# Performance work log

Measured on AMD Instinct MI355X. Metric: run time of the kernel, lower is better.

The kernel has to match this reference:

```python
import jax, jax.numpy as jnp
import numpy as np

NUM_HEADS = 16
HEAD_DIM = 64  # hidden_size 1024 / 16 heads


def setup_inputs() -> dict:
    key = jax.random.key(0)
    ks = jax.random.split(key, 4)
    B, S, H = 2, 2048, 1024
    scale = 1.0 / np.sqrt(H)
    return {
        "hidden_states": jax.random.normal(ks[0], (B, S, H), dtype=jnp.float32),
        "attention_mask": jnp.zeros((B, 1, 1, S), dtype=jnp.float32),
        "Wq": jax.random.normal(ks[1], (H, H), dtype=jnp.float32) * scale,
        "bq": jnp.zeros((H,), dtype=jnp.float32),
        "Wk": jax.random.normal(ks[2], (H, H), dtype=jnp.float32) * scale,
        "bk": jnp.zeros((H,), dtype=jnp.float32),
        "Wv": jax.random.normal(ks[3], (H, H), dtype=jnp.float32) * scale,
        "bv": jnp.zeros((H,), dtype=jnp.float32),
    }


def reference(hidden_states, attention_mask, Wq, bq, Wk, bk, Wv, bv):
    B, S, H = hidden_states.shape
    h, d = NUM_HEADS, HEAD_DIM

    def heads(x):  # [B,S,H] -> [B,h,S,d]
        return x.reshape(B, S, h, d).transpose(0, 2, 1, 3)

    q = heads(hidden_states @ Wq + bq)
    k = heads(hidden_states @ Wk + bk)
    v = heads(hidden_states @ Wv + bv)

    # [B,h,S,S] scores, scaled then additive-masked (HF BERT semantics)
    scores = jnp.einsum("bhqd,bhkd->bhqk", q, k) / jnp.sqrt(jnp.float32(d))
    scores = scores + attention_mask
    probs = jax.nn.softmax(scores, axis=-1)  # dropout p=0 -> identity

    ctx = jnp.einsum("bhqk,bhkd->bhqd", probs, v)
    ctx = ctx.transpose(0, 2, 1, 3).reshape(B, S, H)
    return ctx
```

## Files before the change

kernel.cpp:

```cpp
#include <hip/hip_runtime.h>
#include <hip/hip_bf16.h>


#define SEQ   2048
#define HID   1024
#define NHEAD 16
#define HD    64
#define SD    ((size_t)SEQ * HD)

typedef __bf16 bf16x8 __attribute__((ext_vector_type(8)));
typedef float  f32x4  __attribute__((ext_vector_type(4)));

#define L2E 1.4426950408889634f
#define SOFT_OFF 16.0f

__device__ __forceinline__ unsigned short f2b(float f) {
    unsigned int x = __float_as_uint(f);
    x += 0x7FFFu + ((x >> 16) & 1u);
    return (unsigned short)(x >> 16);
}

__device__ __forceinline__ void gload16(const unsigned short* g,
                                        unsigned short* l) {
    __builtin_amdgcn_global_load_lds(
        (const __attribute__((address_space(1))) unsigned int*)g,
        (__attribute__((address_space(3))) unsigned int*)l, 16, 0, 0);
}

__global__ __launch_bounds__(256) void cvt_x_k(const float* __restrict__ X,
                                               unsigned short* __restrict__ Xb)
{
    const size_t i = ((size_t)blockIdx.x * 256 + threadIdx.x) * 4;
    const float4 v = *(const float4*)(X + i);
    ushort4 o;
    o.x = f2b(v.x); o.y = f2b(v.y); o.z = f2b(v.z); o.w = f2b(v.w);
    *(ushort4*)(Xb + i) = o;
}

__global__ __launch_bounds__(256) void cvt_w_k(
    const float* __restrict__ Wq, const float* __restrict__ Wk,
    const float* __restrict__ Wv, unsigned short* __restrict__ Wtb)
{
    __shared__ __align__(16) unsigned short T[64][68];
    const int z = blockIdx.z;
    const float* __restrict__ W = (z == 0) ? Wq : (z == 1) ? Wk : Wv;
    const int k0 = blockIdx.x * 64, n0 = blockIdx.y * 64;
    const int tid = threadIdx.x;
    #pragma unroll
    for (int it = 0; it < 16; ++it) {
        const int idx = 256 * it + tid;
        const int r = idx >> 6, c = idx & 63;
        T[c][r] = f2b(W[(size_t)(k0 + r) * HID + n0 + c]);
    }
    __syncthreads();
    unsigned short* dst = Wtb + (size_t)z * HID * HID;
    #pragma unroll
    for (int it = 0; it < 4; ++it) {
        const int idx = 256 * it + tid;
        const int n = idx >> 4, c4 = (idx & 15) * 4;
        *(ushort4*)(dst + (size_t)(n0 + n) * HID + k0 + c4) = *(ushort4*)&T[n][c4];
    }
}

__device__ __forceinline__ void gemm_epilogue(
    f32x4 acc[4][4], const float* __restrict__ Bp,
    unsigned short* __restrict__ scratch, unsigned short (*Et)[68],
    int z, int m0, int n0, int wr, int wc, int ln, int quad)
{
    const int b = m0 >> 11;
    const int srow0 = (m0 + wr) & (SEQ - 1);
    const int head = (n0 + wc) >> 6;
    __syncthreads();

    if (z == 2) {
        #pragma unroll
        for (int half = 0; half < 2; ++half) {
            #pragma unroll
            for (int nt2 = 0; nt2 < 2; ++nt2) {
                const int nt = half * 2 + nt2;
                const float bias = Bp[n0 + wc + nt * 16 + ln];
                #pragma unroll
                for (int mt = 0; mt < 4; ++mt) {
                    ushort4 o;
                    o.x = f2b(acc[mt][nt][0] + bias);
                    o.y = f2b(acc[mt][nt][1] + bias);
                    o.z = f2b(acc[mt][nt][2] + bias);
                    o.w = f2b(acc[mt][nt][3] + bias);
                    *(ushort4*)&Et[nt2 * 16 + ln][mt * 16 + quad * 4] = o;
                }
            }
            __syncthreads();
            #pragma unroll
            for (int it = 0; it < 8; ++it) {
                const int d = it * 4 + quad, s4 = ln * 4;
                *(ushort4*)(scratch +
                    ((size_t)(64 + b * NHEAD + head) * HD + half * 32 + d) * SEQ
                    + srow0 + s4) = *(const ushort4*)&Et[d][s4];
            }
            __syncthreads();
        }
    } else {
        #pragma unroll
        for (int half = 0; half < 2; ++half) {
            #pragma unroll
            for (int mt2 = 0; mt2 < 2; ++mt2) {
                const int mt = half * 2 + mt2;
                #pragma unroll
                for (int nt = 0; nt < 4; ++nt) {
                    const float bias = Bp[n0 + wc + nt * 16 + ln];
                    #pragma unroll
                    for (int r = 0; r < 4; ++r)
                        Et[mt2 * 16 + quad * 4 + r][nt * 16 + ln] =
                            f2b(acc[mt][nt][r] + bias);
                }
            }
            __syncthreads();
            #pragma unroll
            for (int it = 0; it < 8; ++it) {
                const int r = it * 4 + quad, c4 = ln * 4;
                *(ushort4*)(scratch +
                    ((size_t)(z * 32 + b * NHEAD + head) * SEQ + srow0
                     + half * 32 + r) * HD + c4) = *(const ushort4*)&Et[r][c4];
            }
            __syncthreads();
        }
    }
}

__global__ __launch_bounds__(256) void qkv_gemm_bf16(
    const unsigned short* __restrict__ Xb, const unsigned short* __restrict__ Wtb,
    const float* __restrict__ bq, const float* __restrict__ bk,
    const float* __restrict__ bv, unsigned short* __restrict__ scratch)
{
    __shared__ __align__(16) unsigned short pool[2][2][128][32];

    const int z = blockIdx.z;
    const float* __restrict__ Bp = (z == 0) ? bq : (z == 1) ? bk : bv;
    const unsigned short* __restrict__ Wz = Wtb + (size_t)z * HID * HID;

    const int tid = threadIdx.x, w = tid >> 6, lane = tid & 63;
    const int ln = lane & 15, quad = lane >> 4;
    const int wr = (w >> 1) * 64, wc = (w & 1) * 64;
    const int m0 = blockIdx.x * 128, n0 = blockIdx.y * 128;

    const int L0 = w * 128 + lane;
    const int r0 = L0 >> 2,        c0 = (L0 & 3) * 8;
    const int r1 = (L0 + 64) >> 2, c1 = ((L0 + 64) & 3) * 8;

    f32x4 acc[4][4];
    #pragma unroll
    for (int i = 0; i < 4; ++i)
        #pragma unroll
        for (int j = 0; j < 4; ++j) acc[i][j] = (f32x4){0.f, 0.f, 0.f, 0.f};

    {
        unsigned short* lx = &pool[0][0][0][0] + (size_t)(w * 128) * 8;
        unsigned short* lw = &pool[0][1][0][0] + (size_t)(w * 128) * 8;
        gload16(Xb + (size_t)(m0 + r0) * HID + c0, lx);
        gload16(Xb + (size_t)(m0 + r1) * HID + c1, lx + 64 * 8);
        gload16(Wz + (size_t)(n0 + r0) * HID + c0, lw);
        gload16(Wz + (size_t)(n0 + r1) * HID + c1, lw + 64 * 8);
    }

    int cur = 0;
    for (int k0 = 0; k0 < HID; k0 += 32) {
        __syncthreads();
        if (k0 + 32 < HID) {
            const int kn = k0 + 32, nxt = cur ^ 1;
            unsigned short* lx = &pool[nxt][0][0][0] + (size_t)(w * 128) * 8;
            unsigned short* lw = &pool[nxt][1][0][0] + (size_t)(w * 128) * 8;
            gload16(Xb + (size_t)(m0 + r0) * HID + kn + c0, lx);
            gload16(Xb + (size_t)(m0 + r1) * HID + kn + c1, lx + 64 * 8);
            gload16(Wz + (size_t)(n0 + r0) * HID + kn + c0, lw);
            gload16(Wz + (size_t)(n0 + r1) * HID + kn + c1, lw + 64 * 8);
        }

        bf16x8 am[4], bn[4];
        #pragma unroll
        for (int t = 0; t < 4; ++t) {
            am[t] = *(const bf16x8*)&pool[cur][0][wr + t * 16 + ln][quad * 8];
            bn[t] = *(const bf16x8*)&pool[cur][1][wc + t * 16 + ln][quad * 8];
        }
        #pragma unroll
        for (int mt = 0; mt < 4; ++mt)
            #pragma unroll
            for (int nt = 0; nt < 4; ++nt)
                acc[mt][nt] = __builtin_amdgcn_mfma_f32_16x16x32_bf16(
                    am[mt], bn[nt], acc[mt][nt], 0, 0, 0);
        cur ^= 1;
    }
    unsigned short (*Et)[68] =
        (unsigned short (*)[68])((unsigned char*)pool + (size_t)w * 4352);
    gemm_epilogue(acc, Bp, scratch, Et, z, m0, n0, wr, wc, ln, quad);
}

__global__ __launch_bounds__(256) void qkv_gemm_fp32(
    const float* __restrict__ X,
    const float* __restrict__ Wq, const float* __restrict__ bq,
    const float* __restrict__ Wk, const float* __restrict__ bk,
    const float* __restrict__ Wv, const float* __restrict__ bv,
    unsigned short* __restrict__ scratch)
{
    __shared__ __align__(16) unsigned char pool[20480];
    unsigned short (*Xs)[40] = (unsigned short (*)[40])pool;
    unsigned short (*Wt)[40] = (unsigned short (*)[40])(pool + 10240);

    const int z = blockIdx.z;
    const float* __restrict__ W  = (z == 0) ? Wq : (z == 1) ? Wk : Wv;
    const float* __restrict__ Bp = (z == 0) ? bq : (z == 1) ? bk : bv;

    const int tid = threadIdx.x, w = tid >> 6, lane = tid & 63;
    const int ln = lane & 15, quad = lane >> 4;
    const int wr = (w >> 1) * 64, wc = (w & 1) * 64;
    const int m0 = blockIdx.x * 128, n0 = blockIdx.y * 128;

    const int xr = tid >> 3, xc = (tid & 7) * 4;
    const int wkr = tid >> 5, wnc = (tid & 31) * 4;

    f32x4 acc[4][4];
    #pragma unroll
    for (int i = 0; i < 4; ++i)
        #pragma unroll
        for (int j = 0; j < 4; ++j) acc[i][j] = (f32x4){0.f, 0.f, 0.f, 0.f};

    for (int k0 = 0; k0 < HID; k0 += 32) {
        __syncthreads();
        #pragma unroll
        for (int it = 0; it < 4; ++it) {
            const int r = xr + 32 * it;
            const float4 xv = *(const float4*)(X + (size_t)(m0 + r) * HID + k0 + xc);
            ushort4 xb;
            xb.x = f2b(xv.x); xb.y = f2b(xv.y); xb.z = f2b(xv.z); xb.w = f2b(xv.w);
            *(ushort4*)&Xs[r][xc] = xb;
            const int kr = wkr + 8 * it;
            const float4 wv = *(const float4*)(W + (size_t)(k0 + kr) * HID + n0 + wnc);
            Wt[wnc + 0][kr] = f2b(wv.x);
            Wt[wnc + 1][kr] = f2b(wv.y);
            Wt[wnc + 2][kr] = f2b(wv.z);
            Wt[wnc + 3][kr] = f2b(wv.w);
        }
        __syncthreads();
        bf16x8 am[4], bn[4];
        #pragma unroll
        for (int t = 0; t < 4; ++t) {
            am[t] = *(const bf16x8*)&Xs[wr + t * 16 + ln][quad * 8];
            bn[t] = *(const bf16x8*)&Wt[wc + t * 16 + ln][quad * 8];
        }
        #pragma unroll
        for (int mt = 0; mt < 4; ++mt)
            #pragma unroll
            for (int nt = 0; nt < 4; ++nt)
                acc[mt][nt] = __builtin_amdgcn_mfma_f32_16x16x32_bf16(
                    am[mt], bn[nt], acc[mt][nt], 0, 0, 0);
    }
    unsigned short (*Et)[68] = (unsigned short (*)[68])(pool + (size_t)w * 4352);
    gemm_epilogue(acc, Bp, scratch, Et, z, m0, n0, wr, wc, ln, quad);
}

__global__ __launch_bounds__(256) void attn_mfma(
    const unsigned short* __restrict__ scratch,
    const float* __restrict__ mask,
    float* __restrict__ out)
{
    __shared__ __align__(16) unsigned char smem[37888];
    unsigned short (*Ks)[64][72] = (unsigned short (*)[64][72])smem;
    unsigned short (*Vt)[64][72] = (unsigned short (*)[64][72])(smem + 18432);
    float* lrbuf = (float*)(smem + 36864);
    float (*OA)[68] = (float (*)[68])smem;
    float (*OB)[68] = (float (*)[68])(smem + 18432);

    const int orig = blockIdx.x;
    const int wg = ((orig & 7) << 7) + (orig >> 3);
    const int qt = wg & 31;
    const int bh = wg >> 5;
    const int b = bh >> 4, head = bh & 15;

    const unsigned short* __restrict__ Qp  = scratch + (size_t)bh * SD;
    const unsigned short* __restrict__ Kp  = scratch + (size_t)(32 + bh) * SD;
    const unsigned short* __restrict__ Vtp = scratch + (size_t)(64 + bh) * SD;
    const float* __restrict__ maskp = mask + b * SEQ;

    const int tid = threadIdx.x, w = tid >> 6, lane = tid & 63;
    const int ln = lane & 15, quad = lane >> 4;
    const int wk0 = w * 16;

    bf16x8 qb[4][2];
    #pragma unroll
    for (int t = 0; t < 4; ++t)
        #pragma unroll
        for (int h = 0; h < 2; ++h)
            qb[t][h] = *(const bf16x8*)(Qp +
                (size_t)(qt * 64 + t * 16 + ln) * HD + h * 32 + quad * 8);

    f32x4 O[4][4];
    #pragma unroll
    for (int i = 0; i < 4; ++i)
        #pragma unroll
        for (int j = 0; j < 4; ++j) O[i][j] = (f32x4){0.f, 0.f, 0.f, 0.f};
    float lr[4] = {0.f, 0.f, 0.f, 0.f};

    const int sr8 = tid >> 3, sc8 = (tid & 7) * 8;

    {
        uint4 a = *(const uint4*)(Kp + (size_t)sr8 * HD + sc8);
        uint4 c = *(const uint4*)(Kp + (size_t)(sr8 + 32) * HD + sc8);
        uint4 d = *(const uint4*)(Vtp + (size_t)sr8 * SEQ + sc8);
        uint4 e = *(const uint4*)(Vtp + (size_t)(sr8 + 32) * SEQ + sc8);
        *(uint4*)&Ks[0][sr8][sc8]      = a;
        *(uint4*)&Ks[0][sr8 + 32][sc8] = c;
        *(uint4*)&Vt[0][sr8][sc8]      = d;
        *(uint4*)&Vt[0][sr8 + 32][sc8] = e;
    }
    uint4 kg0 = *(const uint4*)(Kp + (size_t)(64 + sr8) * HD + sc8);
    uint4 kg1 = *(const uint4*)(Kp + (size_t)(64 + sr8 + 32) * HD + sc8);
    uint4 vg0 = *(const uint4*)(Vtp + (size_t)sr8 * SEQ + 64 + sc8);
    uint4 vg1 = *(const uint4*)(Vtp + (size_t)(sr8 + 32) * SEQ + 64 + sc8);
    __syncthreads();

    const float cc = 0.125f * L2E;

    for (int kt = 0; kt < 32; ++kt) {
        const int cur = kt & 1;
        if (kt < 31) {
            *(uint4*)&Ks[cur ^ 1][sr8][sc8]      = kg0;
            *(uint4*)&Ks[cur ^ 1][sr8 + 32][sc8] = kg1;
            *(uint4*)&Vt[cur ^ 1][sr8][sc8]      = vg0;
            *(uint4*)&Vt[cur ^ 1][sr8 + 32][sc8] = vg1;
        }
        if (kt < 30) {
            const int kn = kt + 2;
            kg0 = *(const uint4*)(Kp + (size_t)(kn * 64 + sr8) * HD + sc8);
            kg1 = *(const uint4*)(Kp + (size_t)(kn * 64 + sr8 + 32) * HD + sc8);
            vg0 = *(const uint4*)(Vtp + (size_t)sr8 * SEQ + kn * 64 + sc8);
            vg1 = *(const uint4*)(Vtp + (size_t)(sr8 + 32) * SEQ + kn * 64 + sc8);
        }

        const bf16x8 ka0 = *(const bf16x8*)&Ks[cur][wk0 + ln][quad * 8];
        const bf16x8 ka1 = *(const bf16x8*)&Ks[cur][wk0 + ln][32 + quad * 8];

        uint2 vl[4];
        #pragma unroll
        for (int dg = 0; dg < 4; ++dg)
            vl[dg] = *(const uint2*)&Vt[cur][dg * 16 + ln][wk0 + quad * 4];

        f32x4 s[4];
        #pragma unroll
        for (int t = 0; t < 4; ++t) {
            f32x4 a = (f32x4){0.f, 0.f, 0.f, 0.f};
            a = __builtin_amdgcn_mfma_f32_16x16x32_bf16(ka0, qb[t][0], a, 0, 0, 0);
            a = __builtin_amdgcn_mfma_f32_16x16x32_bf16(ka1, qb[t][1], a, 0, 0, 0);
            s[t] = a;
        }

        const float4 mk4 = *(const float4*)(maskp + kt * 64 + wk0 + quad * 4);
        const float b0 = fmaf(mk4.x, L2E, -SOFT_OFF);
        const float b1 = fmaf(mk4.y, L2E, -SOFT_OFF);
        const float b2 = fmaf(mk4.z, L2E, -SOFT_OFF);
        const float b3 = fmaf(mk4.w, L2E, -SOFT_OFF);

        bf16x8 pb[4];
        #pragma unroll
        for (int t = 0; t < 4; ++t) {
            const float p0 = exp2f(fmaf(s[t][0], cc, b0));
            const float p1 = exp2f(fmaf(s[t][1], cc, b1));
            const float p2 = exp2f(fmaf(s[t][2], cc, b2));
            const float p3 = exp2f(fmaf(s[t][3], cc, b3));
            lr[t] += (p0 + p1) + (p2 + p3);
            unsigned int w0, w1;
            asm("v_cvt_pk_bf16_f32 %0, %1, %2" : "=v"(w0) : "v"(p0), "v"(p1));
            asm("v_cvt_pk_bf16_f32 %0, %1, %2" : "=v"(w1) : "v"(p2), "v"(p3));
            uint4 pu; pu.x = w0; pu.y = w1; pu.z = w0; pu.w = w1;
            pb[t] = *(bf16x8*)&pu;
        }

        #pragma unroll
        for (int dg = 0; dg < 4; ++dg) {
            uint4 vu; vu.x = vl[dg].x; vu.y = vl[dg].y; vu.z = 0u; vu.w = 0u;
            const bf16x8 va = *(bf16x8*)&vu;
            #pragma unroll
            for (int t = 0; t < 4; ++t)
                O[dg][t] = __builtin_amdgcn_mfma_f32_16x16x32_bf16(
                    va, pb[t], O[dg][t], 0, 0, 0);
        }

        __syncthreads();
    }

    #pragma unroll
    for (int t = 0; t < 4; ++t) {
        lr[t] += __shfl_xor(lr[t], 16);
        lr[t] += __shfl_xor(lr[t], 32);
    }
    if (quad == 0) {
        #pragma unroll
        for (int t = 0; t < 4; ++t) lrbuf[w * 64 + t * 16 + ln] = lr[t];
    }

    #define O_WRITE(BUF) { \
        _Pragma("unroll") for (int dg = 0; dg < 4; ++dg) \
        _Pragma("unroll") for (int t = 0; t < 4; ++t) \
            *(float4*)&BUF[t * 16 + ln][dg * 16 + quad * 4] = \
                *(float4*)&O[dg][t]; }
    #define O_ADD(BUF) { \
        _Pragma("unroll") for (int dg = 0; dg < 4; ++dg) \
        _Pragma("unroll") for (int t = 0; t < 4; ++t) { \
            const float4 x = *(const float4*)&BUF[t * 16 + ln][dg * 16 + quad * 4]; \
            O[dg][t][0] += x.x; O[dg][t][1] += x.y; \
            O[dg][t][2] += x.z; O[dg][t][3] += x.w; } }

    if (w == 1) O_WRITE(OA);
    if (w == 3) O_WRITE(OB);
    __syncthreads();
    if (w == 0) O_ADD(OA);
    if (w == 2) O_ADD(OB);
    __syncthreads();
    if (w == 2) O_WRITE(OA);
    __syncthreads();
    if (w == 0) { O_ADD(OA); O_WRITE(OA); }
    __syncthreads();

    #pragma unroll
    for (int it = 0; it < 4; ++it) {
        const int r = (tid >> 4) + 16 * it, c4 = (tid & 15) * 4;
        const float lrt = lrbuf[r] + lrbuf[64 + r] + lrbuf[128 + r] + lrbuf[192 + r];
        const float inv = 1.0f / lrt;
        float4 v = *(const float4*)&OA[r][c4];
        v.x *= inv; v.y *= inv; v.z *= inv; v.w *= inv;
        *(float4*)(out + ((size_t)b * SEQ + qt * 64 + r) * HID + head * HD + c4) = v;
    }
    #undef O_WRITE
    #undef O_ADD
}

extern "C" void kernel_launch(void* const* d_in, const int* in_sizes, int n_in,
                              void* d_out, int out_size, void* d_ws, size_t ws_size,
                              hipStream_t stream) {
    const float* X    = (const float*)d_in[0];
    const float* mask = (const float*)d_in[1];
    const float* Wq   = (const float*)d_in[2];
    const float* bq   = (const float*)d_in[3];
    const float* Wk   = (const float*)d_in[4];
    const float* bk   = (const float*)d_in[5];
    const float* Wv   = (const float*)d_in[6];
    const float* bv   = (const float*)d_in[7];

    unsigned short* scratch = (unsigned short*)d_ws;
    float* out = (float*)d_out;

    const bool big = (ws_size >= (40ull << 20));
    if (big) {
        unsigned short* Xb  = scratch + 96 * SD;
        unsigned short* Wtb = Xb + (size_t)2 * SEQ * HID;
        cvt_x_k<<<4096, 256, 0, stream>>>(X, Xb);
        cvt_w_k<<<dim3(16, 16, 3), 256, 0, stream>>>(Wq, Wk, Wv, Wtb);
        qkv_gemm_bf16<<<dim3(32, 8, 3), 256, 0, stream>>>(
            Xb, Wtb, bq, bk, bv, scratch);
    } else {
        qkv_gemm_fp32<<<dim3(32, 8, 3), 256, 0, stream>>>(
            X, Wq, bq, Wk, bk, Wv, bv, scratch);
    }
    attn_mfma<<<1024, 256, 0, stream>>>(scratch, mask, out);
}
```

Before: 204.5 us.

## Fuse Q/K/V projections into one GEMM block sharing the X tile

Replaces the per-projection bf16 GEMM (grid z=3, 256 threads) with a single 512-thread kernel that loads each X tile once and multiplies it against all three weight tiles, keeping 3x4x2 accumulators per wave. This cuts X global/LDS traffic by sharing it across Q, K and V, at the cost of more LDS (64KB) and more registers per thread, which can lower occupancy. The epilogue is rewritten per projection: Q and K are written head-major and V is written transposed (d-major).

```diff
diff --git a/kernel.cpp b/kernel.cpp
--- a/kernel.cpp
+++ b/kernel.cpp
@@ -59,6 +59,137 @@
         const int idx = 256 * it + tid;
         const int n = idx >> 4, c4 = (idx & 15) * 4;
         *(ushort4*)(dst + (size_t)(n0 + n) * HID + k0 + c4) = *(ushort4*)&T[n][c4];
+    }
+}
+
+__global__ __launch_bounds__(512) void qkv_gemm_fused(
+    const unsigned short* __restrict__ Xb, const unsigned short* __restrict__ Wtb,
+    const float* __restrict__ bq, const float* __restrict__ bk,
+    const float* __restrict__ bv, unsigned short* __restrict__ scratch)
+{
+    __shared__ __align__(16) unsigned char pool[65536];
+    unsigned short (*Xs)[128][32] = (unsigned short (*)[128][32])pool;
+    unsigned short (*Ws)[3][128][32] = (unsigned short (*)[3][128][32])(pool + 16384);
+
+    const int tid = threadIdx.x, w = tid >> 6, lane = tid & 63;
+    const int ln = lane & 15, quad = lane >> 4;
+    const int wr = (w >> 2) * 64;
+    const int wc = (w & 3) * 32;
+    const int m0 = blockIdx.x * 128, n0 = blockIdx.y * 128;
+
+    const int rS = w * 16 + (lane >> 2);
+    const int cS = (lane & 3) * 8;
+
+    f32x4 acc[3][4][2];
+    #pragma unroll
+    for (int z = 0; z < 3; ++z)
+        #pragma unroll
+        for (int i = 0; i < 4; ++i)
+            #pragma unroll
+            for (int j = 0; j < 2; ++j) acc[z][i][j] = (f32x4){0.f, 0.f, 0.f, 0.f};
+
+    {
+        unsigned short* lx = &Xs[0][0][0] + (size_t)w * 512;
+        gload16(Xb + (size_t)(m0 + rS) * HID + cS, lx);
+        #pragma unroll
+        for (int z = 0; z < 3; ++z) {
+            unsigned short* lw = &Ws[0][z][0][0] + (size_t)w * 512;
+            gload16(Wtb + (size_t)z * HID * HID + (size_t)(n0 + rS) * HID + cS, lw);
+        }
+    }
+
+    int cur = 0;
+    for (int k0 = 0; k0 < HID; k0 += 32) {
+        __syncthreads();
+        if (k0 + 32 < HID) {
+            const int kn = k0 + 32, nxt = cur ^ 1;
+            unsigned short* lx = &Xs[nxt][0][0] + (size_t)w * 512;
+            gload16(Xb + (size_t)(m0 + rS) * HID + kn + cS, lx);
+            #pragma unroll
+            for (int z = 0; z < 3; ++z) {
+                unsigned short* lw = &Ws[nxt][z][0][0] + (size_t)w * 512;
+                gload16(Wtb + (size_t)z * HID * HID + (size_t)(n0 + rS) * HID + kn + cS, lw);
+            }
+        }
+
+        bf16x8 am[4];
+        #pragma unroll
+        for (int t = 0; t < 4; ++t)
+            am[t] = *(const bf16x8*)&Xs[cur][wr + t * 16 + ln][quad * 8];
+        #pragma unroll
+        for (int z = 0; z < 3; ++z) {
+            bf16x8 bn[2];
+            #pragma unroll
+            for (int n = 0; n < 2; ++n)
+                bn[n] = *(const bf16x8*)&Ws[cur][z][wc + n * 16 + ln][quad * 8];
+            #pragma unroll
+            for (int mt = 0; mt < 4; ++mt)
+                #pragma unroll
+                for (int nt = 0; nt < 2; ++nt)
+                    acc[z][mt][nt] = __builtin_amdgcn_mfma_f32_16x16x32_bf16(
+                        am[mt], bn[nt], acc[z][mt][nt], 0, 0, 0);
+        }
+        cur ^= 1;
+    }
+
+    __syncthreads();
+    const int b = m0 >> 11;
+    const int srow0 = (m0 + wr) & (SEQ - 1);
+    const int head = (n0 + wc) >> 6;
+    const int dimb = (n0 + wc) & 63;
+
+    unsigned short (*EtQ)[36] = (unsigned short (*)[36])(pool + (size_t)w * 4352);
+    #pragma unroll
+    for (int z = 0; z < 2; ++z) {
+        const float* __restrict__ Bp = (z == 0) ? bq : bk;
+        float bias[2];
+        #pragma unroll
+        for (int nt = 0; nt < 2; ++nt) bias[nt] = Bp[n0 + wc + nt * 16 + ln];
+        #pragma unroll
+        for (int half = 0; half < 2; ++half) {
+            #pragma unroll
+            for (int mt2 = 0; mt2 < 2; ++mt2) {
+                const int mt = half * 2 + mt2;
+                #pragma unroll
+                for (int nt = 0; nt < 2; ++nt)
+                    #pragma unroll
+                    for (int r = 0; r < 4; ++r)
+                        EtQ[mt2 * 16 + quad * 4 + r][nt * 16 + ln] =
+                            f2b(acc[z][mt][nt][r] + bias[nt]);
+            }
+            #pragma unroll
+            for (int it = 0; it < 4; ++it) {
+                const int row = it * 8 + (lane >> 3), c4 = (lane & 7) * 4;
+                *(ushort4*)(scratch +
+                    ((size_t)(z * 32 + b * NHEAD + head) * SEQ + srow0
+                     + half * 32 + row) * HD + dimb + c4) =
+                    *(const ushort4*)&EtQ[row][c4];
+            }
+        }
+    }
+    {
+        unsigned short (*EtV)[68] = (unsigned short (*)[68])(pool + (size_t)w * 4352);
+        float bias[2];
+        #pragma unroll
+        for (int nt = 0; nt < 2; ++nt) bias[nt] = bv[n0 + wc + nt * 16 + ln];
+        #pragma unroll
+        for (int nt = 0; nt < 2; ++nt)
+            #pragma unroll
+            for (int mt = 0; mt < 4; ++mt) {
+                ushort4 o;
+                o.x = f2b(acc[2][mt][nt][0] + bias[nt]);
+                o.y = f2b(acc[2][mt][nt][1] + bias[nt]);
+                o.z = f2b(acc[2][mt][nt][2] + bias[nt]);
+                o.w = f2b(acc[2][mt][nt][3] + bias[nt]);
+                *(ushort4*)&EtV[nt * 16 + ln][mt * 16 + quad * 4] = o;
+            }
+        #pragma unroll
+        for (int it = 0; it < 8; ++it) {
+            const int d = it * 4 + quad, s4 = ln * 4;
+            *(ushort4*)(scratch +
+                ((size_t)(64 + b * NHEAD + head) * HD + dimb + d) * SEQ
+                + srow0 + s4) = *(const ushort4*)&EtV[d][s4];
+        }
     }
 }
 
@@ -127,73 +258,6 @@
     }
 }
 
-__global__ __launch_bounds__(256) void qkv_gemm_bf16(
-    const unsigned short* __restrict__ Xb, const unsigned short* __restrict__ Wtb,
-    const float* __restrict__ bq, const float* __restrict__ bk,
-    const float* __restrict__ bv, unsigned short* __restrict__ scratch)
-{
-    __shared__ __align__(16) unsigned short pool[2][2][128][32];
-
-    const int z = blockIdx.z;
-    const float* __restrict__ Bp = (z == 0) ? bq : (z == 1) ? bk : bv;
-    const unsigned short* __restrict__ Wz = Wtb + (size_t)z * HID * HID;
-
-    const int tid = threadIdx.x, w = tid >> 6, lane = tid & 63;
-    const int ln = lane & 15, quad = lane >> 4;
-    const int wr = (w >> 1) * 64, wc = (w & 1) * 64;
-    const int m0 = blockIdx.x * 128, n0 = blockIdx.y * 128;
-
-    const int L0 = w * 128 + lane;
-    const int r0 = L0 >> 2,        c0 = (L0 & 3) * 8;
-    const int r1 = (L0 + 64) >> 2, c1 = ((L0 + 64) & 3) * 8;
-
-    f32x4 acc[4][4];
-    #pragma unroll
-    for (int i = 0; i < 4; ++i)
-        #pragma unroll
-        for (int j = 0; j < 4; ++j) acc[i][j] = (f32x4){0.f, 0.f, 0.f, 0.f};
-
-    {
-        unsigned short* lx = &pool[0][0][0][0] + (size_t)(w * 128) * 8;
-        unsigned short* lw = &pool[0][1][0][0] + (size_t)(w * 128) * 8;
-        gload16(Xb + (size_t)(m0 + r0) * HID + c0, lx);
-        gload16(Xb + (size_t)(m0 + r1) * HID + c1, lx + 64 * 8);
-        gload16(Wz + (size_t)(n0 + r0) * HID + c0, lw);
-        gload16(Wz + (size_t)(n0 + r1) * HID + c1, lw + 64 * 8);
-    }
-
-    int cur = 0;
-    for (int k0 = 0; k0 < HID; k0 += 32) {
-        __syncthreads();
-        if (k0 + 32 < HID) {
-            const int kn = k0 + 32, nxt = cur ^ 1;
-            unsigned short* lx = &pool[nxt][0][0][0] + (size_t)(w * 128) * 8;
-            unsigned short* lw = &pool[nxt][1][0][0] + (size_t)(w * 128) * 8;
-            gload16(Xb + (size_t)(m0 + r0) * HID + kn + c0, lx);
-            gload16(Xb + (size_t)(m0 + r1) * HID + kn + c1, lx + 64 * 8);
-            gload16(Wz + (size_t)(n0 + r0) * HID + kn + c0, lw);
-            gload16(Wz + (size_t)(n0 + r1) * HID + kn + c1, lw + 64 * 8);
-        }
-
-        bf16x8 am[4], bn[4];
-        #pragma unroll
-        for (int t = 0; t < 4; ++t) {
-            am[t] = *(const bf16x8*)&pool[cur][0][wr + t * 16 + ln][quad * 8];
-            bn[t] = *(const bf16x8*)&pool[cur][1][wc + t * 16 + ln][quad * 8];
-        }
-        #pragma unroll
-        for (int mt = 0; mt < 4; ++mt)
-            #pragma unroll
-            for (int nt = 0; nt < 4; ++nt)
-                acc[mt][nt] = __builtin_amdgcn_mfma_f32_16x16x32_bf16(
-                    am[mt], bn[nt], acc[mt][nt], 0, 0, 0);
-        cur ^= 1;
-    }
-    unsigned short (*Et)[68] =
-        (unsigned short (*)[68])((unsigned char*)pool + (size_t)w * 4352);
-    gemm_epilogue(acc, Bp, scratch, Et, z, m0, n0, wr, wc, ln, quad);
-}
-
 __global__ __launch_bounds__(256) void qkv_gemm_fp32(
     const float* __restrict__ X,
     const float* __restrict__ Wq, const float* __restrict__ bq,
@@ -453,7 +517,7 @@
         unsigned short* Wtb = Xb + (size_t)2 * SEQ * HID;
         cvt_x_k<<<4096, 256, 0, stream>>>(X, Xb);
         cvt_w_k<<<dim3(16, 16, 3), 256, 0, stream>>>(Wq, Wk, Wv, Wtb);
-        qkv_gemm_bf16<<<dim3(32, 8, 3), 256, 0, stream>>>(
+        qkv_gemm_fused<<<dim3(32, 8), 512, 0, stream>>>(
             Xb, Wtb, bq, bk, bv, scratch);
     } else {
         qkv_gemm_fp32<<<dim3(32, 8, 3), 256, 0, stream>>>(
```

After: 196.0 us. -4.2%, faster.
